# Optimization experiments

Hardware: AMD Instinct MI355X
Metric: run time of the kernel (lower is better)

The kernel has to match this reference:

```python
import jax, jax.numpy as jnp
import numpy as np

B, C, H, W = 8, 8, 640, 640
M = 16  # max instance ids per image (0 = background)
EPS = 1e-12


def setup_inputs() -> dict:
    key = jax.random.key(0)
    k1, k2, k3, k4, k5 = jax.random.split(key, 5)
    outputs = jax.random.normal(k1, (B, C, H, W), dtype=jnp.float32)
    gt_texts = jax.random.randint(k2, (B, H, W), 0, M)
    gt_kernels = jax.random.randint(k3, (B, H, W), 0, M)
    gt_tops = jax.random.randint(k4, (B, H, W), 0, M)
    gt_bots = jax.random.randint(k5, (B, H, W), 0, M)
    return dict(outputs=outputs, gt_texts=gt_texts, gt_kernels=gt_kernels,
                gt_tops=gt_tops, gt_bots=gt_bots)


def _pull_push(outputs, gt_texts, gt_kernels):
    b = outputs.shape[0]
    n = outputs.shape[2] * outputs.shape[3]
    # similarity embedding per pixel: [B, N, 4]
    sim = outputs[:, 4:].reshape(b, 4, n).transpose(0, 2, 1)
    kt = gt_kernels.reshape(b, n)
    tt = gt_texts.reshape(b, n)
    off = jnp.arange(b, dtype=kt.dtype)[:, None] * M
    ids_k = (kt + off).reshape(-1)
    ids_t = (tt + off).reshape(-1)
    sim_flat = sim.reshape(b * n, 4)
    ones = jnp.ones((b * n,), sim.dtype)

    # per-instance kernel centroids G (segment mean over kernel pixels)
    sum_k = jax.ops.segment_sum(sim_flat, ids_k, num_segments=b * M).reshape(b, M, 4)
    cnt_k = jax.ops.segment_sum(ones, ids_k, num_segments=b * M).reshape(b, M)
    G = sum_k / jnp.maximum(cnt_k, 1.0)[..., None]  # [B, M, 4]
    # instance valid iff it has kernel pixels and idx >= 1 (0 is background)
    valid = (cnt_k > 0) & (jnp.arange(M)[None, :] >= 1)

    # pull loss: per text pixel, distance to its instance's kernel centroid
    G_pix = jnp.take_along_axis(G, tt[..., None], axis=1)  # [B, N, 4]
    d = jnp.sqrt(((sim - G_pix) ** 2).sum(-1) + EPS) - 0.5  # [B, N]
    l_pix = jnp.log1p(jnp.maximum(d, 0.0) ** 2).reshape(-1)
    sum_t = jax.ops.segment_sum(l_pix, ids_t, num_segments=b * M).reshape(b, M)
    cnt_t = jax.ops.segment_sum(ones, ids_t, num_segments=b * M).reshape(b, M)
    per_inst = sum_t / jnp.maximum(cnt_t, 1.0)  # mean over each instance's text pixels
    nv = valid.sum(-1).astype(sim.dtype)
    loss_pull = (per_inst * valid).sum(-1) / jnp.maximum(nv, 1.0)

    # push loss: pairwise centroid separation, pairs (i < j) of valid instances
    diff = G[:, :, None, :] - G[:, None, :, :]  # [B, M, M, 4]
    dk = jnp.sqrt((diff ** 2).sum(-1) + EPS)
    val = jnp.log1p(jnp.maximum(3.0 - dk, 0.0) ** 2)
    iu = jnp.triu(jnp.ones((M, M), bool), 1)
    pm = valid[:, :, None] & valid[:, None, :] & iu[None]
    push_sum = (val * pm).sum((1, 2))
    denom = nv * (nv - 1.0)  # matches original normalization n*(n-1)
    loss_push = jnp.where(nv > 1, push_sum / jnp.maximum(denom, 1.0), 0.0)
    return loss_pull, loss_push


def reference(outputs, gt_texts, gt_kernels, gt_tops, gt_bots):
    # gt_tops/gt_bots are consumed by broken (non-contributing) branches in the
    # original code; the returned losses depend only on gt_texts/gt_kernels.
    return _pull_push(outputs, gt_texts, gt_kernels)
```

## Files before the change

kernel.cpp:

```cpp
#include <hip/hip_runtime.h>
#include <math.h>

#define BB 8
#define MI 16
#define NN 409600
#define CEPS 1e-12f
#define GPB 64
#define TPB 256
#define CHUNKS 400

#define WS_SUM  0
#define WS_CNTK 512
#define WS_ST   640
#define WS_CNTT 768
#define WS_G    896
#define WS_VAL  1408
#define WS_ZERO_FLOATS 896

#define VALK(v) ((v) < 16 ? a0[(v) & 15] : (v) < 32 ? a1[(v) & 15] \
               : (v) < 48 ? a2[(v) & 15] : a3[(v) & 15])

__global__ __launch_bounds__(TPB) void k_sums(
    const float* __restrict__ outputs, const int* __restrict__ gt_kernels,
    float* __restrict__ ws) {
  __shared__ float red[TPB * 36];
  __shared__ unsigned int scnt[MI];
  const int b = blockIdx.y;
  const int tid = threadIdx.x;
  if (tid < MI) scnt[tid] = 0u;
  __syncthreads();

  float a0[MI], a1[MI], a2[MI], a3[MI];
  unsigned int wcnt[MI];
#pragma unroll
  for (int m = 0; m < MI; m++) { a0[m] = 0.f; a1[m] = 0.f; a2[m] = 0.f; a3[m] = 0.f; wcnt[m] = 0u; }

  const float* s0 = outputs + (size_t)(b * 8 + 4) * NN;
  const int* gkb = gt_kernels + (size_t)b * NN;

  for (int c = blockIdx.x; c < CHUNKS; c += GPB) {
    const int pix = c * 1024 + tid * 4;
    const int4 id4 = *(const int4*)(gkb + pix);
    const float4 x0 = *(const float4*)(s0 + pix);
    const float4 x1 = *(const float4*)(s0 + NN + pix);
    const float4 x2 = *(const float4*)(s0 + 2 * NN + pix);
    const float4 x3 = *(const float4*)(s0 + 3 * NN + pix);
#define SLOTK(IDC, XC)                                                       \
    {                                                                        \
      const int id = id4.IDC;                                                \
      _Pragma("unroll")                                                      \
      for (int m = 0; m < MI; m++) {                                         \
        const bool e = (id == m);                                            \
        wcnt[m] += (unsigned)__popcll(__ballot(e));                          \
        const float f = e ? 1.f : 0.f;                                       \
        a0[m] += f * x0.XC; a1[m] += f * x1.XC;                              \
        a2[m] += f * x2.XC; a3[m] += f * x3.XC;                              \
      }                                                                      \
    }
    SLOTK(x, x) SLOTK(y, y) SLOTK(z, z) SLOTK(w, w)
#undef SLOTK
  }

  if ((tid & 63) == 0) {
#pragma unroll
    for (int m = 0; m < MI; m++) atomicAdd(&scnt[m], wcnt[m]);
  }

#pragma unroll
  for (int r = 0; r < 2; r++) {
    __syncthreads();
#pragma unroll
    for (int j = 0; j < 32; j++) red[tid * 36 + j] = VALK(r * 32 + j);
    __syncthreads();
    const int m = tid & 31, grp = tid >> 5;
    float p = 0.f;
#pragma unroll
    for (int k = 0; k < 32; k++) p += red[(grp * 32 + k) * 36 + m];
    __syncthreads();
    red[grp * 36 + m] = p;
    __syncthreads();
    if (tid < 32) {
      float t = 0.f;
#pragma unroll
      for (int g = 0; g < 8; g++) t += red[g * 36 + tid];
      atomicAdd(&ws[WS_SUM + b * 64 + r * 32 + tid], t);
    }
  }
  __syncthreads();
  if (tid < MI) atomicAdd(&((int*)ws)[WS_CNTK + b * MI + tid], (int)scnt[tid]);
}

__global__ void k_finalize_G(float* __restrict__ ws) {
  const int j = threadIdx.x;
  if (j >= BB * MI) return;
  const int b = j >> 4, m = j & 15;
  const int cnt = ((const int*)ws)[WS_CNTK + j];
  const float inv = 1.f / fmaxf((float)cnt, 1.f);
  ws[WS_G + j * 4 + 0] = ws[WS_SUM + b * 64 + 0 * 16 + m] * inv;
  ws[WS_G + j * 4 + 1] = ws[WS_SUM + b * 64 + 1 * 16 + m] * inv;
  ws[WS_G + j * 4 + 2] = ws[WS_SUM + b * 64 + 2 * 16 + m] * inv;
  ws[WS_G + j * 4 + 3] = ws[WS_SUM + b * 64 + 3 * 16 + m] * inv;
  ws[WS_VAL + j] = (cnt > 0 && m >= 1) ? 1.f : 0.f;
}

__global__ __launch_bounds__(TPB) void k_pull(
    const float* __restrict__ outputs, const int* __restrict__ gt_texts,
    float* __restrict__ ws) {
  __shared__ float red[TPB * 20];
  __shared__ unsigned int scnt[MI];
  __shared__ float4 sG[MI];
  const int b = blockIdx.y;
  const int tid = threadIdx.x;
  if (tid < MI) {
    scnt[tid] = 0u;
    sG[tid] = ((const float4*)(ws + WS_G))[b * MI + tid];
  }
  __syncthreads();

  float al[MI];
  unsigned int wcnt[MI];
#pragma unroll
  for (int m = 0; m < MI; m++) { al[m] = 0.f; wcnt[m] = 0u; }

  const float* s0 = outputs + (size_t)(b * 8 + 4) * NN;
  const int* ttb = gt_texts + (size_t)b * NN;

  for (int c = blockIdx.x; c < CHUNKS; c += GPB) {
    const int pix = c * 1024 + tid * 4;
    const int4 id4 = *(const int4*)(ttb + pix);
    const float4 x0 = *(const float4*)(s0 + pix);
    const float4 x1 = *(const float4*)(s0 + NN + pix);
    const float4 x2 = *(const float4*)(s0 + 2 * NN + pix);
    const float4 x3 = *(const float4*)(s0 + 3 * NN + pix);
#define SLOTP(IDC, XC)                                                       \
    {                                                                        \
      const int id = id4.IDC;                                                \
      const float4 g = sG[id];                                               \
      const float d0 = x0.XC - g.x, d1 = x1.XC - g.y;                        \
      const float d2 = x2.XC - g.z, d3 = x3.XC - g.w;                        \
      const float dist = sqrtf(d0*d0 + d1*d1 + d2*d2 + d3*d3 + CEPS) - 0.5f; \
      const float dm = fmaxf(dist, 0.f);                                     \
      const float l = log1pf(dm * dm);                                       \
      _Pragma("unroll")                                                      \
      for (int m = 0; m < MI; m++) {                                         \
        const bool e = (id == m);                                            \
        wcnt[m] += (unsigned)__popcll(__ballot(e));                          \
        al[m] += (e ? 1.f : 0.f) * l;                                        \
      }                                                                      \
    }
    SLOTP(x, x) SLOTP(y, y) SLOTP(z, z) SLOTP(w, w)
#undef SLOTP
  }

  if ((tid & 63) == 0) {
#pragma unroll
    for (int m = 0; m < MI; m++) atomicAdd(&scnt[m], wcnt[m]);
  }

  __syncthreads();
#pragma unroll
  for (int j = 0; j < MI; j++) red[tid * 20 + j] = al[j];
  __syncthreads();
  const int m = tid & 15, grp = tid >> 4;
  float p = 0.f;
#pragma unroll
  for (int k = 0; k < 16; k++) p += red[(grp * 16 + k) * 20 + m];
  __syncthreads();
  red[grp * 20 + m] = p;
  __syncthreads();
  if (tid < MI) {
    float t = 0.f;
#pragma unroll
    for (int g = 0; g < 16; g++) t += red[g * 20 + tid];
    atomicAdd(&ws[WS_ST + b * MI + tid], t);
    atomicAdd(&((int*)ws)[WS_CNTT + b * MI + tid], (int)scnt[tid]);
  }
}

__global__ void k_final(const float* __restrict__ ws, float* __restrict__ out) {
  const int b = threadIdx.x;
  if (b >= BB) return;
  const float* G = ws + WS_G;
  const float* valid = ws + WS_VAL;
  float nv = 0.f;
  for (int m = 0; m < MI; m++) nv += valid[b * MI + m];
  float pull = 0.f;
  for (int m = 0; m < MI; m++) {
    const int j = b * MI + m;
    const float cnt = (float)((const int*)ws)[WS_CNTT + j];
    const float per = ws[WS_ST + j] / fmaxf(cnt, 1.f);
    pull += per * valid[j];
  }
  pull /= fmaxf(nv, 1.f);
  float push = 0.f;
  for (int i = 0; i < MI; i++) {
    if (valid[b * MI + i] == 0.f) continue;
    for (int j = i + 1; j < MI; j++) {
      if (valid[b * MI + j] == 0.f) continue;
      float d2 = CEPS;
      for (int c = 0; c < 4; c++) {
        const float df = G[(b * MI + i) * 4 + c] - G[(b * MI + j) * 4 + c];
        d2 += df * df;
      }
      const float dk = sqrtf(d2);
      const float t = fmaxf(3.f - dk, 0.f);
      push += log1pf(t * t);
    }
  }
  const float denom = nv * (nv - 1.f);
  push = (nv > 1.f) ? push / fmaxf(denom, 1.f) : 0.f;
  out[b] = pull;
  out[BB + b] = push;
}

extern "C" void kernel_launch(void* const* d_in, const int* in_sizes, int n_in,
                              void* d_out, int out_size, void* d_ws, size_t ws_size,
                              hipStream_t stream) {
  const float* outputs = (const float*)d_in[0];
  const int* gt_texts = (const int*)d_in[1];
  const int* gt_kernels = (const int*)d_in[2];
  float* ws = (float*)d_ws;
  float* out = (float*)d_out;

  hipMemsetAsync(d_ws, 0, WS_ZERO_FLOATS * sizeof(float), stream);

  dim3 grid(GPB, BB);
  k_sums<<<grid, TPB, 0, stream>>>(outputs, gt_kernels, ws);
  k_finalize_G<<<1, 128, 0, stream>>>(ws);
  k_pull<<<grid, TPB, 0, stream>>>(outputs, gt_texts, ws);
  k_final<<<1, 64, 0, stream>>>(ws, out);
}
```

Before: 254.2 us.

## Replace global atomics with per-block partials and deterministic two-stage reduction

Each block now handles a fixed contiguous 4096-pixel tile (grid widened to 100 blocks per image) and writes its per-instance partial sums and counts to a workspace slot instead of doing global atomicAdds. The finalize kernels reduce these partials, so the memset is no longer needed. The aim is to drop the atomic contention and the memset launch and to spread load across more blocks. The cost is a larger workspace, extra reduction work in the finalize kernels, and counts now accumulated in float.

```diff
diff --git a/kernel.cpp b/kernel.cpp
--- a/kernel.cpp
+++ b/kernel.cpp
@@ -5,17 +5,13 @@
 #define MI 16
 #define NN 409600
 #define CEPS 1e-12f
-#define GPB 64
+#define GPB 100
 #define TPB 256
-#define CHUNKS 400
-
-#define WS_SUM  0
-#define WS_CNTK 512
-#define WS_ST   640
-#define WS_CNTT 768
-#define WS_G    896
-#define WS_VAL  1408
-#define WS_ZERO_FLOATS 896
+
+#define WS_PS   0
+#define WS_G    (BB*80*GPB)
+#define WS_VAL  (WS_G + BB*MI*4)
+#define WS_PP   (WS_VAL + BB*MI)
 
 #define VALK(v) ((v) < 16 ? a0[(v) & 15] : (v) < 32 ? a1[(v) & 15] \
                : (v) < 48 ? a2[(v) & 15] : a3[(v) & 15])
@@ -24,11 +20,9 @@
     const float* __restrict__ outputs, const int* __restrict__ gt_kernels,
     float* __restrict__ ws) {
   __shared__ float red[TPB * 36];
-  __shared__ unsigned int scnt[MI];
-  const int b = blockIdx.y;
-  const int tid = threadIdx.x;
-  if (tid < MI) scnt[tid] = 0u;
-  __syncthreads();
+  __shared__ float cw[4 * MI];
+  __shared__ float outbuf[80];
+  const int b = blockIdx.y, blk = blockIdx.x, tid = threadIdx.x;
 
   float a0[MI], a1[MI], a2[MI], a3[MI];
   unsigned int wcnt[MI];
@@ -37,9 +31,11 @@
 
   const float* s0 = outputs + (size_t)(b * 8 + 4) * NN;
   const int* gkb = gt_kernels + (size_t)b * NN;
-
-  for (int c = blockIdx.x; c < CHUNKS; c += GPB) {
-    const int pix = c * 1024 + tid * 4;
+  const int base = blk * 4096;
+
+#pragma unroll
+  for (int c = 0; c < 4; c++) {
+    const int pix = base + c * 1024 + tid * 4;
     const int4 id4 = *(const int4*)(gkb + pix);
     const float4 x0 = *(const float4*)(s0 + pix);
     const float4 x1 = *(const float4*)(s0 + NN + pix);
@@ -62,8 +58,9 @@
   }
 
   if ((tid & 63) == 0) {
-#pragma unroll
-    for (int m = 0; m < MI; m++) atomicAdd(&scnt[m], wcnt[m]);
+    const int w = tid >> 6;
+#pragma unroll
+    for (int m = 0; m < MI; m++) cw[w * MI + m] = (float)wcnt[m];
   }
 
 #pragma unroll
@@ -83,38 +80,51 @@
       float t = 0.f;
 #pragma unroll
       for (int g = 0; g < 8; g++) t += red[g * 36 + tid];
-      atomicAdd(&ws[WS_SUM + b * 64 + r * 32 + tid], t);
-    }
-  }
-  __syncthreads();
-  if (tid < MI) atomicAdd(&((int*)ws)[WS_CNTK + b * MI + tid], (int)scnt[tid]);
-}
-
-__global__ void k_finalize_G(float* __restrict__ ws) {
-  const int j = threadIdx.x;
-  if (j >= BB * MI) return;
-  const int b = j >> 4, m = j & 15;
-  const int cnt = ((const int*)ws)[WS_CNTK + j];
-  const float inv = 1.f / fmaxf((float)cnt, 1.f);
-  ws[WS_G + j * 4 + 0] = ws[WS_SUM + b * 64 + 0 * 16 + m] * inv;
-  ws[WS_G + j * 4 + 1] = ws[WS_SUM + b * 64 + 1 * 16 + m] * inv;
-  ws[WS_G + j * 4 + 2] = ws[WS_SUM + b * 64 + 2 * 16 + m] * inv;
-  ws[WS_G + j * 4 + 3] = ws[WS_SUM + b * 64 + 3 * 16 + m] * inv;
-  ws[WS_VAL + j] = (cnt > 0 && m >= 1) ? 1.f : 0.f;
+      outbuf[r * 32 + tid] = t;
+    }
+  }
+  __syncthreads();
+  if (tid < MI)
+    outbuf[64 + tid] = cw[tid] + cw[MI + tid] + cw[2 * MI + tid] + cw[3 * MI + tid];
+  __syncthreads();
+  if (tid < 80) ws[WS_PS + (b * 80 + tid) * GPB + blk] = outbuf[tid];
+}
+
+__global__ void k_finG(float* __restrict__ ws) {
+  __shared__ float part[4 * 80];
+  __shared__ float tot[80];
+  const int b = blockIdx.x, t = threadIdx.x;
+  const int v = t % 80, h = t / 80;
+  float s = 0.f;
+  const float* src = ws + WS_PS + (b * 80 + v) * GPB + h * 25;
+#pragma unroll 5
+  for (int k = 0; k < 25; k++) s += src[k];
+  part[h * 80 + v] = s;
+  __syncthreads();
+  if (t < 80) tot[t] = part[t] + part[80 + t] + part[160 + t] + part[240 + t];
+  __syncthreads();
+  if (t < MI) {
+    const float cnt = tot[64 + t];
+    const float inv = 1.f / fmaxf(cnt, 1.f);
+    float4 g;
+    g.x = tot[0 * 16 + t] * inv;
+    g.y = tot[1 * 16 + t] * inv;
+    g.z = tot[2 * 16 + t] * inv;
+    g.w = tot[3 * 16 + t] * inv;
+    ((float4*)(ws + WS_G))[b * MI + t] = g;
+    ws[WS_VAL + b * MI + t] = (cnt > 0.f && t >= 1) ? 1.f : 0.f;
+  }
 }
 
 __global__ __launch_bounds__(TPB) void k_pull(
     const float* __restrict__ outputs, const int* __restrict__ gt_texts,
     float* __restrict__ ws) {
   __shared__ float red[TPB * 20];
-  __shared__ unsigned int scnt[MI];
+  __shared__ float cw[4 * MI];
+  __shared__ float outbuf[32];
   __shared__ float4 sG[MI];
-  const int b = blockIdx.y;
-  const int tid = threadIdx.x;
-  if (tid < MI) {
-    scnt[tid] = 0u;
-    sG[tid] = ((const float4*)(ws + WS_G))[b * MI + tid];
-  }
+  const int b = blockIdx.y, blk = blockIdx.x, tid = threadIdx.x;
+  if (tid < MI) sG[tid] = ((const float4*)(ws + WS_G))[b * MI + tid];
   __syncthreads();
 
   float al[MI];
@@ -124,9 +134,11 @@
 
   const float* s0 = outputs + (size_t)(b * 8 + 4) * NN;
   const int* ttb = gt_texts + (size_t)b * NN;
-
-  for (int c = blockIdx.x; c < CHUNKS; c += GPB) {
-    const int pix = c * 1024 + tid * 4;
+  const int base = blk * 4096;
+
+#pragma unroll
+  for (int c = 0; c < 4; c++) {
+    const int pix = base + c * 1024 + tid * 4;
     const int4 id4 = *(const int4*)(ttb + pix);
     const float4 x0 = *(const float4*)(s0 + pix);
     const float4 x1 = *(const float4*)(s0 + NN + pix);
@@ -153,8 +165,9 @@
   }
 
   if ((tid & 63) == 0) {
-#pragma unroll
-    for (int m = 0; m < MI; m++) atomicAdd(&scnt[m], wcnt[m]);
+    const int w = tid >> 6;
+#pragma unroll
+    for (int m = 0; m < MI; m++) cw[w * MI + m] = (float)wcnt[m];
   }
 
   __syncthreads();
@@ -172,45 +185,55 @@
     float t = 0.f;
 #pragma unroll
     for (int g = 0; g < 16; g++) t += red[g * 20 + tid];
-    atomicAdd(&ws[WS_ST + b * MI + tid], t);
-    atomicAdd(&((int*)ws)[WS_CNTT + b * MI + tid], (int)scnt[tid]);
-  }
+    outbuf[tid] = t;
+    outbuf[MI + tid] = cw[tid] + cw[MI + tid] + cw[2 * MI + tid] + cw[3 * MI + tid];
+  }
+  __syncthreads();
+  if (tid < 32) ws[WS_PP + (b * 32 + tid) * GPB + blk] = outbuf[tid];
 }
 
 __global__ void k_final(const float* __restrict__ ws, float* __restrict__ out) {
-  const int b = threadIdx.x;
-  if (b >= BB) return;
-  const float* G = ws + WS_G;
-  const float* valid = ws + WS_VAL;
-  float nv = 0.f;
-  for (int m = 0; m < MI; m++) nv += valid[b * MI + m];
-  float pull = 0.f;
-  for (int m = 0; m < MI; m++) {
-    const int j = b * MI + m;
-    const float cnt = (float)((const int*)ws)[WS_CNTT + j];
-    const float per = ws[WS_ST + j] / fmaxf(cnt, 1.f);
-    pull += per * valid[j];
-  }
-  pull /= fmaxf(nv, 1.f);
-  float push = 0.f;
-  for (int i = 0; i < MI; i++) {
-    if (valid[b * MI + i] == 0.f) continue;
-    for (int j = i + 1; j < MI; j++) {
-      if (valid[b * MI + j] == 0.f) continue;
-      float d2 = CEPS;
-      for (int c = 0; c < 4; c++) {
-        const float df = G[(b * MI + i) * 4 + c] - G[(b * MI + j) * 4 + c];
-        d2 += df * df;
+  __shared__ float tot[256];
+  const int t = threadIdx.x;
+  const int b = t >> 5, v = t & 31;
+  float s = 0.f;
+  const float* src = ws + WS_PP + (b * 32 + v) * GPB;
+#pragma unroll 4
+  for (int k = 0; k < GPB; k++) s += src[k];
+  tot[t] = s;
+  __syncthreads();
+  if (t < BB) {
+    const int bb = t;
+    const float* G = ws + WS_G;
+    const float* valid = ws + WS_VAL;
+    float nv = 0.f;
+    for (int m = 0; m < MI; m++) nv += valid[bb * MI + m];
+    float pull = 0.f;
+    for (int m = 0; m < MI; m++) {
+      const float per = tot[bb * 32 + m] / fmaxf(tot[bb * 32 + 16 + m], 1.f);
+      pull += per * valid[bb * MI + m];
+    }
+    pull /= fmaxf(nv, 1.f);
+    float push = 0.f;
+    for (int i = 0; i < MI; i++) {
+      if (valid[bb * MI + i] == 0.f) continue;
+      for (int j = i + 1; j < MI; j++) {
+        if (valid[bb * MI + j] == 0.f) continue;
+        float d2 = CEPS;
+        for (int c = 0; c < 4; c++) {
+          const float df = G[(bb * MI + i) * 4 + c] - G[(bb * MI + j) * 4 + c];
+          d2 += df * df;
+        }
+        const float dk = sqrtf(d2);
+        const float tt = fmaxf(3.f - dk, 0.f);
+        push += log1pf(tt * tt);
       }
-      const float dk = sqrtf(d2);
-      const float t = fmaxf(3.f - dk, 0.f);
-      push += log1pf(t * t);
-    }
-  }
-  const float denom = nv * (nv - 1.f);
-  push = (nv > 1.f) ? push / fmaxf(denom, 1.f) : 0.f;
-  out[b] = pull;
-  out[BB + b] = push;
+    }
+    const float denom = nv * (nv - 1.f);
+    push = (nv > 1.f) ? push / fmaxf(denom, 1.f) : 0.f;
+    out[bb] = pull;
+    out[BB + bb] = push;
+  }
 }
 
 extern "C" void kernel_launch(void* const* d_in, const int* in_sizes, int n_in,
@@ -222,11 +245,9 @@
   float* ws = (float*)d_ws;
   float* out = (float*)d_out;
 
-  hipMemsetAsync(d_ws, 0, WS_ZERO_FLOATS * sizeof(float), stream);
-
   dim3 grid(GPB, BB);
   k_sums<<<grid, TPB, 0, stream>>>(outputs, gt_kernels, ws);
-  k_finalize_G<<<1, 128, 0, stream>>>(ws);
+  k_finG<<<BB, 320, 0, stream>>>(ws);
   k_pull<<<grid, TPB, 0, stream>>>(outputs, gt_texts, ws);
-  k_final<<<1, 64, 0, stream>>>(ws, out);
-}
+  k_final<<<1, 256, 0, stream>>>(ws, out);
+}
```

New measurement: 316.0 us. +24.3%, slower.
